# Kernel tuning notes

Hardware: AMD Instinct MI355X
Metric: run time of the kernel (lower is better)

## Reference

```python
import jax, jax.numpy as jnp
import numpy as np

B, T, IN = 256, 512, 4      # batch, seq_len, input dim
M, D, NS = 3, 256, 64       # n kaarma models, dictionary size, state dim
H = 128                     # controller (GRU) hidden size
GU, GS = 0.5, 0.5           # gaussian kernel widths (input / state)


def setup_inputs() -> dict:
    key = jax.random.key(0)
    ks = jax.random.split(key, 12)
    s = lambda k, shp, sc: (jax.random.normal(k, shp, dtype=jnp.float32) * sc)
    return {
        "x": s(ks[0], (B, T, IN), 1.0),
        "y": s(ks[1], (B, T), 1.0),
        # MKAARMA: per-model dictionary (inputs U, states S) and coefficients A
        "U": s(ks[2], (M, D, IN), 1.0),
        "S": s(ks[3], (M, D, NS), 0.3),
        "A": s(ks[4], (M, D, NS), 1.0 / np.sqrt(D)),
        # GRU controller (input dim = M + 1 error channel)
        "W_ih": s(ks[5], (M + 1, 3 * H), 1.0 / np.sqrt(M + 1)),
        "W_hh": s(ks[6], (H, 3 * H), 1.0 / np.sqrt(H)),
        "b_ih": s(ks[7], (3 * H,), 0.1),
        "b_hh": s(ks[8], (3 * H,), 0.1),
        # linear_decode: (H-1) -> M gate logits
        "Wd": s(ks[9], (H - 1, M), 1.0 / np.sqrt(H - 1)),
        "bd": s(ks[10], (M,), 0.1),
    }


def _forward(x, y, U, S, A, W_ih, W_hh, b_ih, b_hh, Wd, bd):
    init_gate = jnp.array([[0.3333, 0.3333, 0.3334]], dtype=x.dtype)

    def step(carry, xs):
        s, h, gate_prev, err = carry          # [B,NS], [B,H], [B,M], [B]
        x_t, y_t = xs                         # [B,IN], [B]
        # --- mkaarma: gaussian input*state kernel against dictionary ---
        du = jnp.sum((x_t[:, None, None, :] - U[None]) ** 2, axis=-1)  # [B,M,D]
        ds = jnp.sum((s[:, None, None, :] - S[None]) ** 2, axis=-1)   # [B,M,D]
        K = jnp.exp(-GU * du - GS * ds)                                # [B,M,D]
        new_state = jnp.einsum('bmd,mdn->bmn', K, A)                   # [B,M,NS]
        encoded = jnp.max(K, axis=-1)                                  # [B,M]
        # --- controller: GRU cell on [similarities, error] ---
        inp = jnp.concatenate([encoded, err[:, None]], axis=1)         # [B,M+1]
        gi = inp @ W_ih + b_ih
        gh = h @ W_hh + b_hh
        ir, iz, inn = jnp.split(gi, 3, axis=1)
        hr, hz, hn = jnp.split(gh, 3, axis=1)
        r = jax.nn.sigmoid(ir + hr)
        z = jax.nn.sigmoid(iz + hz)
        n = jnp.tanh(inn + r * hn)
        h_new = (1.0 - z) * n + z * h                                  # [B,H]
        # --- gate decode + theta blend ---
        gate = jax.nn.softmax(h_new[:, :-1] @ Wd + bd, axis=1)          # [B,M]
        theta = jax.nn.sigmoid(h_new[:, -1:])                           # [B,1]
        gate = gate * theta + gate_prev * (1.0 - theta)
        s_new = jnp.einsum('bm,bmn->bn', gate, new_state)               # [B,NS]
        pred = s_new[:, -1]                                             # [B]
        err_new = pred - y_t
        penalty = jnp.sum(gate * (1.0 - gate), axis=1, keepdims=True)   # [B,1]
        return (s_new, h_new, gate, err_new), (pred, penalty)

    carry0 = (
        jnp.zeros((x.shape[0], NS), x.dtype),
        jnp.zeros((x.shape[0], H), x.dtype),
        jnp.tile(init_gate, (x.shape[0], 1)),
        jnp.ones((x.shape[0],), x.dtype),
    )
    xs = (jnp.swapaxes(x, 0, 1), jnp.swapaxes(y, 0, 1))  # time-major
    _, (o, p) = jax.lax.scan(step, carry0, xs)
    return jnp.swapaxes(o, 0, 1), jnp.swapaxes(p, 0, 1)   # [B,T], [B,T,1]


def reference(x, y, U, S, A, W_ih, W_hh, b_ih, b_hh, Wd, bd):
    return _forward(x, y, U, S, A, W_ih, W_hh, b_ih, b_hh, Wd, bd)
```

## Files before the change

kernel.cpp:

```cpp
#include <hip/hip_runtime.h>
#include <math.h>

constexpr int kB  = 256;
constexpr int kT  = 512;
constexpr int kNS = 64;
constexpr int kH  = 128;

constexpr int kWRowsLds = 256;
constexpr int kWPad     = 132;

__device__ __forceinline__ float sigmoidf_(float v) { return 1.0f / (1.0f + __expf(-v)); }
__device__ __forceinline__ float dot4(float4 a, float4 b) {
    return a.x*b.x + a.y*b.y + a.z*b.z + a.w*b.w;
}

template <int CTRL>
__device__ __forceinline__ float dppf(float x) {
    return __int_as_float(__builtin_amdgcn_mov_dpp(__float_as_int(x), CTRL, 0xf, 0xf, true));
}
__device__ __forceinline__ float red_max64(float x) {
    x = fmaxf(x, dppf<0xB1>(x));
    x = fmaxf(x, dppf<0x4E>(x));
    x = fmaxf(x, dppf<0x124>(x));
    x = fmaxf(x, dppf<0x128>(x));
    x = fmaxf(x, __shfl_xor(x, 16, 64));
    x = fmaxf(x, __shfl_xor(x, 32, 64));
    return x;
}
__device__ __forceinline__ float red_sum64(float x) {
    x += dppf<0xB1>(x);
    x += dppf<0x4E>(x);
    x += dppf<0x124>(x);
    x += dppf<0x128>(x);
    x += __shfl_xor(x, 16, 64);
    x += __shfl_xor(x, 32, 64);
    return x;
}

extern "C" __global__ void __launch_bounds__(256)
whh_transpose(const float* __restrict__ Whh, float* __restrict__ WhhT) {
    const int o = blockIdx.x * 256 + threadIdx.x;
    const int j = o >> 7, k = o & 127;
    WhhT[o] = Whh[k * 384 + j];
}

extern "C" __global__ void __launch_bounds__(512, 2)
disc_kernel(const float* __restrict__ x,   const float* __restrict__ y,
            const float* __restrict__ U,   const float* __restrict__ S,
            const float* __restrict__ A,   const float* __restrict__ Wih,
            const float* __restrict__ bih, const float* __restrict__ bhh,
            const float* __restrict__ Wd,  const float* __restrict__ bd,
            const float* __restrict__ WhhT,
            float* __restrict__ out_o,  float* __restrict__ out_p)
{
    const int b    = blockIdx.x;
    const int tid  = threadIdx.x;
    const int lane = tid & 63;
    const int wid  = tid >> 6;
    const int hb   = tid & 1;

    __shared__ __align__(16) float sh_K[768];
    __shared__ __align__(16) float sh_part[512];
    __shared__ __align__(16) float sh_part2[512];
    __shared__ __align__(16) float sh_gh[384];
    __shared__ __align__(16) float sh_h[2][kH];
    __shared__ __align__(16) float sh_s[kNS];
    __shared__ __align__(16) float sh_Wih[4 * 384];
    __shared__ __align__(16) float sh_bih[384];
    __shared__ __align__(16) float sh_bhh[384];
    __shared__ float sh_Wd[384];
    __shared__ float sh_bd[4];
    __shared__ float sh_encA[8];
    __shared__ float sh_encB[8];
    __shared__ __align__(16) float sh_xt[4];
    __shared__ float sh_x2, sh_s2, sh_err;
    __shared__ float sh_yt[2];
    __shared__ __align__(16) float sh_W[kWRowsLds * kWPad];

    const float4* S4 = reinterpret_cast<const float4*>(S);
    const float4* U4 = reinterpret_cast<const float4*>(U);

    float4 Sa[16]; float4 Ua; float Ca;
    float4 Sb[8];  float Ub0, Ub1; float Cb;
    {
        float ss = 0.f;
#pragma unroll
        for (int j = 0; j < 16; ++j) { Sa[j] = S4[tid * 16 + j]; ss += dot4(Sa[j], Sa[j]); }
        Ua = U4[tid];
        Ca = -0.5f * (dot4(Ua, Ua) + ss);
    }
    const int pbrow = 512 + (tid >> 1);
    {
        float ss = 0.f;
#pragma unroll
        for (int j = 0; j < 8; ++j) { Sb[j] = S4[pbrow * 16 + hb * 8 + j]; ss += dot4(Sb[j], Sb[j]); }
        Ub0 = U[pbrow * 4 + hb * 2 + 0];
        Ub1 = U[pbrow * 4 + hb * 2 + 1];
        Cb = -0.5f * (Ub0*Ub0 + Ub1*Ub1 + ss);
    }
    float A1[64];
#pragma unroll
    for (int dd = 0; dd < 64; ++dd)
        A1[dd] = A[((wid >> 2) * 256 + (wid & 3) * 64 + dd) * 64 + lane];
    float A2[32];
#pragma unroll
    for (int dd = 0; dd < 32; ++dd)
        A2[dd] = A[(512 + (wid >> 1) * 64 + (wid & 1) * 32 + dd) * 64 + lane];

    float g0 = 0.3333f, g1 = 0.3333f, g2 = 0.3334f;

    for (int i = tid; i < 1536; i += 512) sh_Wih[i] = Wih[i];
    for (int i = tid; i < 384; i += 512) {
        sh_bih[i] = bih[i];
        sh_bhh[i] = bhh[i];
        sh_gh[i]  = bhh[i];
        sh_Wd[i]  = (i < 381) ? Wd[i] : 0.f;
    }
    for (int i4 = tid; i4 < kWRowsLds * 32; i4 += 512) {
        const int r = i4 >> 5, c4 = i4 & 31;
        reinterpret_cast<float4*>(sh_W + r * kWPad)[c4] =
            reinterpret_cast<const float4*>(WhhT)[i4];
    }
    if (tid < 3) sh_bd[tid] = bd[tid];
    if (tid < kNS) sh_s[tid] = 0.f;
    if (tid < kH)  { sh_h[0][tid] = 0.f; sh_h[1][tid] = 0.f; }
    if (tid == 0) {
        sh_err = 1.0f; sh_s2 = 0.f;
        float4 xv = reinterpret_cast<const float4*>(x)[(size_t)b * kT];
        reinterpret_cast<float4*>(sh_xt)[0] = xv;
        sh_x2 = dot4(xv, xv);
        sh_yt[0] = y[(size_t)b * kT];
    }
    __syncthreads();

    for (int t = 0; t < kT; ++t) {
        const int par  = t & 1;
        const int par1 = (t + 1) & 1;

        if (wid >= 1 && wid <= 4) {
            const int u = tid - 64;
            const float4* W4 = reinterpret_cast<const float4*>(sh_W + u * kWPad);
            const float4* h4 = reinterpret_cast<const float4*>(sh_h[par]);
            float g = 0.f;
#pragma unroll 4
            for (int k4 = 16; k4 < 32; ++k4)
                g += dot4(h4[k4], W4[k4]);
            sh_gh[u] += g;
        } else if (wid == 5 || wid == 6) {
            const int u = 256 + (tid - 320);
            const float4* W4 = reinterpret_cast<const float4*>(WhhT) + u * 32;
            const float4* h4 = reinterpret_cast<const float4*>(sh_h[par]);
            float g = 0.f;
#pragma unroll 4
            for (int k4 = 24; k4 < 32; ++k4)
                g += dot4(h4[k4], W4[k4]);
            sh_gh[u] += g;
        }
        {
            const float scal = -0.5f * (sh_x2 + sh_s2);
            const float4 xt4 = reinterpret_cast<const float4*>(sh_xt)[0];
            const float4* s4 = reinterpret_cast<const float4*>(sh_s);
            float da0 = 0.f, da1 = 0.f, dblo = 0.f, dbhi = 0.f;
#pragma unroll
            for (int j = 0; j < 8; ++j) {
                const float4 sv0 = s4[j];
                const float4 sv1 = s4[8 + j];
                da0  += dot4(sv0, Sa[j]);
                da1  += dot4(sv1, Sa[8 + j]);
                dblo += dot4(sv0, Sb[j]);
                dbhi += dot4(sv1, Sb[j]);
            }
            const float db = hb ? dbhi : dblo;
            const float kk_a = __expf(scal + Ca + dot4(xt4, Ua) + da0 + da1);
            const float xbp  = hb ? (xt4.z*Ub0 + xt4.w*Ub1) : (xt4.x*Ub0 + xt4.y*Ub1);
            const float ph   = db + Cb + xbp;
            const float po   = dppf<0xB1>(ph);
            const float kk_b = __expf(scal + ph + po);
            sh_K[tid] = kk_a;
            if (hb == 0) sh_K[512 + (tid >> 1)] = kk_b;
            const float mA = red_max64(kk_a);
            const float mB = red_max64(kk_b);
            if (lane == 0) { sh_encA[wid] = mA; sh_encB[wid] = mB; }
        }
        __syncthreads();

        {
            const float4* K4 = reinterpret_cast<const float4*>(sh_K + wid * 64);
            float acc = 0.f;
#pragma unroll
            for (int j = 0; j < 16; ++j) {
                const float4 kv = K4[j];
                acc += kv.x*A1[4*j] + kv.y*A1[4*j+1] + kv.z*A1[4*j+2] + kv.w*A1[4*j+3];
            }
            sh_part[tid] = acc;
            const float4* K4b = reinterpret_cast<const float4*>(
                                    sh_K + 512 + (wid >> 1) * 64 + (wid & 1) * 32);
            float accb = 0.f;
#pragma unroll
            for (int j = 0; j < 8; ++j) {
                const float4 kv = K4b[j];
                accb += kv.x*A2[4*j] + kv.y*A2[4*j+1] + kv.z*A2[4*j+2] + kv.w*A2[4*j+3];
            }
            sh_part2[tid] = accb;
        }
        if (tid < 128) {
            const float e0 = fmaxf(fmaxf(sh_encA[0], sh_encA[1]), fmaxf(sh_encA[2], sh_encA[3]));
            const float e1 = fmaxf(fmaxf(sh_encA[4], sh_encA[5]), fmaxf(sh_encA[6], sh_encA[7]));
            const float e2 = fmaxf(fmaxf(fmaxf(sh_encB[0], sh_encB[1]), fmaxf(sh_encB[2], sh_encB[3])),
                                   fmaxf(fmaxf(sh_encB[4], sh_encB[5]), fmaxf(sh_encB[6], sh_encB[7])));
            const float er = sh_err;
            const int j = tid;
            const float gir = sh_bih[j]       + e0*sh_Wih[j]        + e1*sh_Wih[384 + j]
                                              + e2*sh_Wih[768 + j]  + er*sh_Wih[1152 + j];
            const float giz = sh_bih[128 + j] + e0*sh_Wih[128 + j]  + e1*sh_Wih[512 + j]
                                              + e2*sh_Wih[896 + j]  + er*sh_Wih[1280 + j];
            const float gin = sh_bih[256 + j] + e0*sh_Wih[256 + j]  + e1*sh_Wih[640 + j]
                                              + e2*sh_Wih[1024 + j] + er*sh_Wih[1408 + j];
            const float r  = sigmoidf_(gir + sh_gh[j]);
            const float z  = sigmoidf_(giz + sh_gh[128 + j]);
            const float nn = tanhf(gin + r * sh_gh[256 + j]);
            sh_h[par1][j] = (1.f - z) * nn + z * sh_h[par][j];
        }
        __syncthreads();

        if (wid == 0) {
            const float hA = sh_h[par1][lane];
            const float hB = sh_h[par1][64 + lane];
            const float theta = sigmoidf_(sh_h[par1][127]);
            float l0 = hA * sh_Wd[lane*3+0] + hB * sh_Wd[(64+lane)*3+0];
            float l1 = hA * sh_Wd[lane*3+1] + hB * sh_Wd[(64+lane)*3+1];
            float l2 = hA * sh_Wd[lane*3+2] + hB * sh_Wd[(64+lane)*3+2];
            l0 = red_sum64(l0);
            l1 = red_sum64(l1);
            l2 = red_sum64(l2);
            l0 += sh_bd[0]; l1 += sh_bd[1]; l2 += sh_bd[2];
            const float mx = fmaxf(l0, fmaxf(l1, l2));
            const float x0 = __expf(l0 - mx), x1 = __expf(l1 - mx), x2 = __expf(l2 - mx);
            const float inv = theta / (x0 + x1 + x2);
            const float omt = 1.f - theta;
            g0 = x0*inv + g0*omt;
            g1 = x1*inv + g1*omt;
            g2 = x2*inv + g2*omt;
            const float ns0 = (sh_part[lane]       + sh_part[64 + lane])
                            + (sh_part[128 + lane] + sh_part[192 + lane]);
            const float ns1 = (sh_part[256 + lane] + sh_part[320 + lane])
                            + (sh_part[384 + lane] + sh_part[448 + lane]);
            const float ns2 = ((sh_part2[lane]       + sh_part2[64 + lane])
                            +  (sh_part2[128 + lane] + sh_part2[192 + lane]))
                            + ((sh_part2[256 + lane] + sh_part2[320 + lane])
                            +  (sh_part2[384 + lane] + sh_part2[448 + lane]));
            const float sn = g0*ns0 + g1*ns1 + g2*ns2;
            sh_s[lane] = sn;
            if (lane == 0)
                out_p[(size_t)b * kT + t] = g0*(1.f-g0) + g1*(1.f-g1) + g2*(1.f-g2);
            if (lane == 63) {
                out_o[(size_t)b * kT + t] = sn;
                sh_err = sn - sh_yt[par];
            }
            const float ss = red_sum64(sn * sn);
            if (lane == 0) sh_s2 = ss;
        } else if (wid <= 4) {
            const int u = tid - 64;
            const float4* W4 = reinterpret_cast<const float4*>(sh_W + u * kWPad);
            const float4* h4 = reinterpret_cast<const float4*>(sh_h[par1]);
            float g = sh_bhh[u];
#pragma unroll 8
            for (int k4 = 0; k4 < 16; ++k4)
                g += dot4(h4[k4], W4[k4]);
            sh_gh[u] = g;
        } else if (wid <= 6) {
            const int u = 256 + (tid - 320);
            const float4* W4 = reinterpret_cast<const float4*>(WhhT) + u * 32;
            const float4* h4 = reinterpret_cast<const float4*>(sh_h[par1]);
            float g = sh_bhh[u];
#pragma unroll 8
            for (int k4 = 0; k4 < 24; ++k4)
                g += dot4(h4[k4], W4[k4]);
            sh_gh[u] = g;
        } else {
            if (lane == 0 && (t + 1) < kT) {
                float4 xv = reinterpret_cast<const float4*>(x)[(size_t)b * kT + t + 1];
                reinterpret_cast<float4*>(sh_xt)[0] = xv;
                sh_x2 = dot4(xv, xv);
                sh_yt[par1] = y[(size_t)b * kT + t + 1];
            }
        }
        __syncthreads();
    }
}

extern "C" void kernel_launch(void* const* d_in, const int* in_sizes, int n_in,
                              void* d_out, int out_size, void* d_ws, size_t ws_size,
                              hipStream_t stream)
{
    const float* x   = (const float*)d_in[0];
    const float* y   = (const float*)d_in[1];
    const float* U   = (const float*)d_in[2];
    const float* S   = (const float*)d_in[3];
    const float* A   = (const float*)d_in[4];
    const float* Wih = (const float*)d_in[5];
    const float* Whh = (const float*)d_in[6];
    const float* bih = (const float*)d_in[7];
    const float* bhh = (const float*)d_in[8];
    const float* Wd  = (const float*)d_in[9];
    const float* bd  = (const float*)d_in[10];

    float* WhhT  = (float*)d_ws;
    float* out_o = (float*)d_out;
    float* out_p = out_o + kB * kT;

    hipLaunchKernelGGL(whh_transpose, dim3(192), dim3(256), 0, stream, Whh, WhhT);
    hipLaunchKernelGGL(disc_kernel, dim3(kB), dim3(512), 0, stream,
                       x, y, U, S, A, Wih, bih, bhh, Wd, bd, WhhT, out_o, out_p);
}
```

Before: 2.655 ms.

## Widen block to 768 threads, one dictionary entry per thread, simplify GRU split

```diff
diff --git a/kernel.cpp b/kernel.cpp
--- a/kernel.cpp
+++ b/kernel.cpp
@@ -5,6 +5,7 @@
 constexpr int kT  = 512;
 constexpr int kNS = 64;
 constexpr int kH  = 128;
+constexpr int kNT = 768;
 
 constexpr int kWRowsLds = 256;
 constexpr int kWPad     = 132;
@@ -44,7 +45,7 @@
     WhhT[o] = Whh[k * 384 + j];
 }
 
-extern "C" __global__ void __launch_bounds__(512, 2)
+extern "C" __global__ void __launch_bounds__(768, 3)
 disc_kernel(const float* __restrict__ x,   const float* __restrict__ y,
             const float* __restrict__ U,   const float* __restrict__ S,
             const float* __restrict__ A,   const float* __restrict__ Wih,
@@ -57,21 +58,19 @@
     const int tid  = threadIdx.x;
     const int lane = tid & 63;
     const int wid  = tid >> 6;
-    const int hb   = tid & 1;
 
     __shared__ __align__(16) float sh_K[768];
-    __shared__ __align__(16) float sh_part[512];
-    __shared__ __align__(16) float sh_part2[512];
-    __shared__ __align__(16) float sh_gh[384];
-    __shared__ __align__(16) float sh_h[2][kH];
+    __shared__ __align__(16) float sh_part[768];
+    __shared__ __align__(16) float sh_gh[256];
+    __shared__ __align__(16) float sh_ghn[2][128];
+    __shared__ __align__(16) float sh_h[kH];
     __shared__ __align__(16) float sh_s[kNS];
     __shared__ __align__(16) float sh_Wih[4 * 384];
     __shared__ __align__(16) float sh_bih[384];
     __shared__ __align__(16) float sh_bhh[384];
     __shared__ float sh_Wd[384];
     __shared__ float sh_bd[4];
-    __shared__ float sh_encA[8];
-    __shared__ float sh_encB[8];
+    __shared__ float sh_enc[12];
     __shared__ __align__(16) float sh_xt[4];
     __shared__ float sh_x2, sh_s2, sh_err;
     __shared__ float sh_yt[2];
@@ -81,7 +80,6 @@
     const float4* U4 = reinterpret_cast<const float4*>(U);
 
     float4 Sa[16]; float4 Ua; float Ca;
-    float4 Sb[8];  float Ub0, Ub1; float Cb;
     {
         float ss = 0.f;
 #pragma unroll
@@ -89,41 +87,28 @@
         Ua = U4[tid];
         Ca = -0.5f * (dot4(Ua, Ua) + ss);
     }
-    const int pbrow = 512 + (tid >> 1);
-    {
-        float ss = 0.f;
-#pragma unroll
-        for (int j = 0; j < 8; ++j) { Sb[j] = S4[pbrow * 16 + hb * 8 + j]; ss += dot4(Sb[j], Sb[j]); }
-        Ub0 = U[pbrow * 4 + hb * 2 + 0];
-        Ub1 = U[pbrow * 4 + hb * 2 + 1];
-        Cb = -0.5f * (Ub0*Ub0 + Ub1*Ub1 + ss);
-    }
     float A1[64];
 #pragma unroll
     for (int dd = 0; dd < 64; ++dd)
-        A1[dd] = A[((wid >> 2) * 256 + (wid & 3) * 64 + dd) * 64 + lane];
-    float A2[32];
-#pragma unroll
-    for (int dd = 0; dd < 32; ++dd)
-        A2[dd] = A[(512 + (wid >> 1) * 64 + (wid & 1) * 32 + dd) * 64 + lane];
+        A1[dd] = A[(wid * 64 + dd) * 64 + lane];
 
     float g0 = 0.3333f, g1 = 0.3333f, g2 = 0.3334f;
 
-    for (int i = tid; i < 1536; i += 512) sh_Wih[i] = Wih[i];
-    for (int i = tid; i < 384; i += 512) {
+    for (int i = tid; i < 1536; i += kNT) sh_Wih[i] = Wih[i];
+    for (int i = tid; i < 384; i += kNT) {
         sh_bih[i] = bih[i];
         sh_bhh[i] = bhh[i];
-        sh_gh[i]  = bhh[i];
         sh_Wd[i]  = (i < 381) ? Wd[i] : 0.f;
     }
-    for (int i4 = tid; i4 < kWRowsLds * 32; i4 += 512) {
+    for (int i = tid; i < 256; i += kNT) sh_gh[i] = bhh[i];
+    if (tid < 128) { sh_ghn[0][tid] = 0.f; sh_ghn[1][tid] = 0.f; sh_h[tid] = 0.f; }
+    for (int i4 = tid; i4 < kWRowsLds * 32; i4 += kNT) {
         const int r = i4 >> 5, c4 = i4 & 31;
         reinterpret_cast<float4*>(sh_W + r * kWPad)[c4] =
             reinterpret_cast<const float4*>(WhhT)[i4];
     }
     if (tid < 3) sh_bd[tid] = bd[tid];
     if (tid < kNS) sh_s[tid] = 0.f;
-    if (tid < kH)  { sh_h[0][tid] = 0.f; sh_h[1][tid] = 0.f; }
     if (tid == 0) {
         sh_err = 1.0f; sh_s2 = 0.f;
         float4 xv = reinterpret_cast<const float4*>(x)[(size_t)b * kT];
@@ -137,77 +122,38 @@
         const int par  = t & 1;
         const int par1 = (t + 1) & 1;
 
-        if (wid >= 1 && wid <= 4) {
-            const int u = tid - 64;
-            const float4* W4 = reinterpret_cast<const float4*>(sh_W + u * kWPad);
-            const float4* h4 = reinterpret_cast<const float4*>(sh_h[par]);
-            float g = 0.f;
-#pragma unroll 4
-            for (int k4 = 16; k4 < 32; ++k4)
-                g += dot4(h4[k4], W4[k4]);
-            sh_gh[u] += g;
-        } else if (wid == 5 || wid == 6) {
-            const int u = 256 + (tid - 320);
-            const float4* W4 = reinterpret_cast<const float4*>(WhhT) + u * 32;
-            const float4* h4 = reinterpret_cast<const float4*>(sh_h[par]);
-            float g = 0.f;
-#pragma unroll 4
-            for (int k4 = 24; k4 < 32; ++k4)
-                g += dot4(h4[k4], W4[k4]);
-            sh_gh[u] += g;
-        }
         {
             const float scal = -0.5f * (sh_x2 + sh_s2);
             const float4 xt4 = reinterpret_cast<const float4*>(sh_xt)[0];
             const float4* s4 = reinterpret_cast<const float4*>(sh_s);
-            float da0 = 0.f, da1 = 0.f, dblo = 0.f, dbhi = 0.f;
+            float da0 = 0.f, da1 = 0.f;
 #pragma unroll
             for (int j = 0; j < 8; ++j) {
-                const float4 sv0 = s4[j];
-                const float4 sv1 = s4[8 + j];
-                da0  += dot4(sv0, Sa[j]);
-                da1  += dot4(sv1, Sa[8 + j]);
-                dblo += dot4(sv0, Sb[j]);
-                dbhi += dot4(sv1, Sb[j]);
-            }
-            const float db = hb ? dbhi : dblo;
-            const float kk_a = __expf(scal + Ca + dot4(xt4, Ua) + da0 + da1);
-            const float xbp  = hb ? (xt4.z*Ub0 + xt4.w*Ub1) : (xt4.x*Ub0 + xt4.y*Ub1);
-            const float ph   = db + Cb + xbp;
-            const float po   = dppf<0xB1>(ph);
-            const float kk_b = __expf(scal + ph + po);
-            sh_K[tid] = kk_a;
-            if (hb == 0) sh_K[512 + (tid >> 1)] = kk_b;
-            const float mA = red_max64(kk_a);
-            const float mB = red_max64(kk_b);
-            if (lane == 0) { sh_encA[wid] = mA; sh_encB[wid] = mB; }
+                da0 += dot4(s4[j],     Sa[j]);
+                da1 += dot4(s4[8 + j], Sa[8 + j]);
+            }
+            const float kk = __expf(scal + Ca + dot4(xt4, Ua) + da0 + da1);
+            sh_K[tid] = kk;
+            const float m = red_max64(kk);
+            if (lane == 0) sh_enc[wid] = m;
         }
         __syncthreads();
 
         {
             const float4* K4 = reinterpret_cast<const float4*>(sh_K + wid * 64);
-            float acc = 0.f;
-#pragma unroll
-            for (int j = 0; j < 16; ++j) {
-                const float4 kv = K4[j];
-                acc += kv.x*A1[4*j] + kv.y*A1[4*j+1] + kv.z*A1[4*j+2] + kv.w*A1[4*j+3];
-            }
-            sh_part[tid] = acc;
-            const float4* K4b = reinterpret_cast<const float4*>(
-                                    sh_K + 512 + (wid >> 1) * 64 + (wid & 1) * 32);
-            float accb = 0.f;
-#pragma unroll
-            for (int j = 0; j < 8; ++j) {
-                const float4 kv = K4b[j];
-                accb += kv.x*A2[4*j] + kv.y*A2[4*j+1] + kv.z*A2[4*j+2] + kv.w*A2[4*j+3];
-            }
-            sh_part2[tid] = accb;
+            float acc0 = 0.f, acc1 = 0.f;
+#pragma unroll
+            for (int j = 0; j < 16; j += 2) {
+                const float4 k0 = K4[j], k1 = K4[j + 1];
+                acc0 += k0.x*A1[4*j]   + k0.y*A1[4*j+1] + k0.z*A1[4*j+2] + k0.w*A1[4*j+3];
+                acc1 += k1.x*A1[4*j+4] + k1.y*A1[4*j+5] + k1.z*A1[4*j+6] + k1.w*A1[4*j+7];
+            }
+            sh_part[tid] = acc0 + acc1;
         }
         if (tid < 128) {
-            const float e0 = fmaxf(fmaxf(sh_encA[0], sh_encA[1]), fmaxf(sh_encA[2], sh_encA[3]));
-            const float e1 = fmaxf(fmaxf(sh_encA[4], sh_encA[5]), fmaxf(sh_encA[6], sh_encA[7]));
-            const float e2 = fmaxf(fmaxf(fmaxf(sh_encB[0], sh_encB[1]), fmaxf(sh_encB[2], sh_encB[3])),
-                                   fmaxf(fmaxf(sh_encB[4], sh_encB[5]), fmaxf(sh_encB[6], sh_encB[7])));
+            const float e0 = fmaxf(fmaxf(sh_enc[0], sh_enc[1]),  fmaxf(sh_enc[2],  sh_enc[3]));
+            const float e1 = fmaxf(fmaxf(sh_enc[4], sh_enc[5]),  fmaxf(sh_enc[6],  sh_enc[7]));
+            const float e2 = fmaxf(fmaxf(sh_enc[8], sh_enc[9]),  fmaxf(sh_enc[10], sh_enc[11]));
             const float er = sh_err;
             const int j = tid;
             const float gir = sh_bih[j]       + e0*sh_Wih[j]        + e1*sh_Wih[384 + j]
@@ -216,17 +162,18 @@
                                               + e2*sh_Wih[896 + j]  + er*sh_Wih[1280 + j];
             const float gin = sh_bih[256 + j] + e0*sh_Wih[256 + j]  + e1*sh_Wih[640 + j]
                                               + e2*sh_Wih[1024 + j] + er*sh_Wih[1408 + j];
+            const float hn_ = sh_bhh[256 + j] + sh_ghn[0][j] + sh_ghn[1][j];
             const float r  = sigmoidf_(gir + sh_gh[j]);
             const float z  = sigmoidf_(giz + sh_gh[128 + j]);
-            const float nn = tanhf(gin + r * sh_gh[256 + j]);
-            sh_h[par1][j] = (1.f - z) * nn + z * sh_h[par][j];
+            const float nn = tanhf(gin + r * hn_);
+            sh_h[j] = (1.f - z) * nn + z * sh_h[j];
         }
         __syncthreads();
 
         if (wid == 0) {
-            const float hA = sh_h[par1][lane];
-            const float hB = sh_h[par1][64 + lane];
-            const float theta = sigmoidf_(sh_h[par1][127]);
+            const float hA = sh_h[lane];
+            const float hB = sh_h[64 + lane];
+            const float theta = sigmoidf_(sh_h[127]);
             float l0 = hA * sh_Wd[lane*3+0] + hB * sh_Wd[(64+lane)*3+0];
             float l1 = hA * sh_Wd[lane*3+1] + hB * sh_Wd[(64+lane)*3+1];
             float l2 = hA * sh_Wd[lane*3+2] + hB * sh_Wd[(64+lane)*3+2];
@@ -245,10 +192,8 @@
                             + (sh_part[128 + lane] + sh_part[192 + lane]);
             const float ns1 = (sh_part[256 + lane] + sh_part[320 + lane])
                             + (sh_part[384 + lane] + sh_part[448 + lane]);
-            const float ns2 = ((sh_part2[lane]       + sh_part2[64 + lane])
-                            +  (sh_part2[128 + lane] + sh_part2[192 + lane]))
-                            + ((sh_part2[256 + lane] + sh_part2[320 + lane])
-                            +  (sh_part2[384 + lane] + sh_part2[448 + lane]));
+            const float ns2 = (sh_part[512 + lane] + sh_part[576 + lane])
+                            + (sh_part[640 + lane] + sh_part[704 + lane]);
             const float sn = g0*ns0 + g1*ns1 + g2*ns2;
             sh_s[lane] = sn;
             if (lane == 0)
@@ -259,31 +204,37 @@
             }
             const float ss = red_sum64(sn * sn);
             if (lane == 0) sh_s2 = ss;
-        } else if (wid <= 4) {
-            const int u = tid - 64;
-            const float4* W4 = reinterpret_cast<const float4*>(sh_W + u * kWPad);
-            const float4* h4 = reinterpret_cast<const float4*>(sh_h[par1]);
-            float g = sh_bhh[u];
-#pragma unroll 8
-            for (int k4 = 0; k4 < 16; ++k4)
-                g += dot4(h4[k4], W4[k4]);
-            sh_gh[u] = g;
-        } else if (wid <= 6) {
-            const int u = 256 + (tid - 320);
-            const float4* W4 = reinterpret_cast<const float4*>(WhhT) + u * 32;
-            const float4* h4 = reinterpret_cast<const float4*>(sh_h[par1]);
-            float g = sh_bhh[u];
-#pragma unroll 8
-            for (int k4 = 0; k4 < 24; ++k4)
-                g += dot4(h4[k4], W4[k4]);
-            sh_gh[u] = g;
-        } else {
+        } else if (wid == 1) {
             if (lane == 0 && (t + 1) < kT) {
                 float4 xv = reinterpret_cast<const float4*>(x)[(size_t)b * kT + t + 1];
                 reinterpret_cast<float4*>(sh_xt)[0] = xv;
                 sh_x2 = dot4(xv, xv);
                 sh_yt[par1] = y[(size_t)b * kT + t + 1];
             }
+        } else if (wid < 6) {
+            const int u = tid - 128;
+            const float4* W4 = reinterpret_cast<const float4*>(sh_W + u * kWPad);
+            const float4* h4 = reinterpret_cast<const float4*>(sh_h);
+            float ga = sh_bhh[u], gb = 0.f;
+#pragma unroll 8
+            for (int k4 = 0; k4 < 32; k4 += 2) {
+                ga += dot4(h4[k4],     W4[k4]);
+                gb += dot4(h4[k4 + 1], W4[k4 + 1]);
+            }
+            sh_gh[u] = ga + gb;
+        } else if (wid < 10) {
+            const int v    = tid - 384;
+            const int u    = 256 + (v >> 1);
+            const int half = v & 1;
+            const float4* W4 = reinterpret_cast<const float4*>(WhhT) + u * 32 + half * 16;
+            const float4* h4 = reinterpret_cast<const float4*>(sh_h) + half * 16;
+            float ga = 0.f, gb = 0.f;
+#pragma unroll 8
+            for (int k4 = 0; k4 < 16; k4 += 2) {
+                ga += dot4(h4[k4],     W4[k4]);
+                gb += dot4(h4[k4 + 1], W4[k4 + 1]);
+            }
+            sh_ghn[half][u - 256] = ga + gb;
         }
         __syncthreads();
     }
@@ -310,6 +261,6 @@
     float* out_p = out_o + kB * kT;
 
     hipLaunchKernelGGL(whh_transpose, dim3(192), dim3(256), 0, stream, Whh, WhhT);
-    hipLaunchKernelGGL(disc_kernel, dim3(kB), dim3(512), 0, stream,
+    hipLaunchKernelGGL(disc_kernel, dim3(kB), dim3(kNT), 0, stream,
                        x, y, U, S, A, Wih, bih, bhh, Wd, bd, WhhT, out_o, out_p);
 }
```

New measurement: 2.672 ms. Within noise of the previous version (+0.6%).

## Replicate gate/state tail across warps to drop one barrier per timestep

Applied to the files above, without the earlier changes.

```diff
diff --git a/kernel.cpp b/kernel.cpp
--- a/kernel.cpp
+++ b/kernel.cpp
@@ -10,6 +10,9 @@
 constexpr int kWPad     = 132;
 
 __device__ __forceinline__ float sigmoidf_(float v) { return 1.0f / (1.0f + __expf(-v)); }
+__device__ __forceinline__ float tanhf_(float v) {
+    return 1.0f - 2.0f / (1.0f + __expf(2.0f * v));
+}
 __device__ __forceinline__ float dot4(float4 a, float4 b) {
     return a.x*b.x + a.y*b.y + a.z*b.z + a.w*b.w;
 }
@@ -63,8 +66,8 @@
     __shared__ __align__(16) float sh_part[512];
     __shared__ __align__(16) float sh_part2[512];
     __shared__ __align__(16) float sh_gh[384];
-    __shared__ __align__(16) float sh_h[2][kH];
-    __shared__ __align__(16) float sh_s[kNS];
+    __shared__ __align__(16) float sh_h[kH];
+    __shared__ __align__(16) float sh_sW[8][kNS];
     __shared__ __align__(16) float sh_Wih[4 * 384];
     __shared__ __align__(16) float sh_bih[384];
     __shared__ __align__(16) float sh_bhh[384];
@@ -72,8 +75,7 @@
     __shared__ float sh_bd[4];
     __shared__ float sh_encA[8];
     __shared__ float sh_encB[8];
-    __shared__ __align__(16) float sh_xt[4];
-    __shared__ float sh_x2, sh_s2, sh_err;
+    __shared__ __align__(16) float sh_xt[2][4];
     __shared__ float sh_yt[2];
     __shared__ __align__(16) float sh_W[kWRowsLds * kWPad];
 
@@ -108,6 +110,7 @@
         A2[dd] = A[(512 + (wid >> 1) * 64 + (wid & 1) * 32 + dd) * 64 + lane];
 
     float g0 = 0.3333f, g1 = 0.3333f, g2 = 0.3334f;
+    float err = 1.0f, s2 = 0.f;
 
     for (int i = tid; i < 1536; i += 512) sh_Wih[i] = Wih[i];
     for (int i = tid; i < 384; i += 512) {
@@ -121,45 +124,62 @@
         reinterpret_cast<float4*>(sh_W + r * kWPad)[c4] =
             reinterpret_cast<const float4*>(WhhT)[i4];
     }
+    sh_sW[wid][lane] = 0.f;
     if (tid < 3) sh_bd[tid] = bd[tid];
-    if (tid < kNS) sh_s[tid] = 0.f;
-    if (tid < kH)  { sh_h[0][tid] = 0.f; sh_h[1][tid] = 0.f; }
+    if (tid < kH) sh_h[tid] = 0.f;
     if (tid == 0) {
-        sh_err = 1.0f; sh_s2 = 0.f;
         float4 xv = reinterpret_cast<const float4*>(x)[(size_t)b * kT];
-        reinterpret_cast<float4*>(sh_xt)[0] = xv;
-        sh_x2 = dot4(xv, xv);
+        reinterpret_cast<float4*>(sh_xt[0])[0] = xv;
         sh_yt[0] = y[(size_t)b * kT];
     }
     __syncthreads();
 
+    auto tail_step = [&](int tp) {
+        const float hA = sh_h[lane];
+        const float hB = sh_h[64 + lane];
+        const float theta = sigmoidf_(sh_h[127]);
+        float l0 = hA * sh_Wd[lane*3+0] + hB * sh_Wd[(64+lane)*3+0];
+        float l1 = hA * sh_Wd[lane*3+1] + hB * sh_Wd[(64+lane)*3+1];
+        float l2 = hA * sh_Wd[lane*3+2] + hB * sh_Wd[(64+lane)*3+2];
+        l0 = red_sum64(l0) + sh_bd[0];
+        l1 = red_sum64(l1) + sh_bd[1];
+        l2 = red_sum64(l2) + sh_bd[2];
+        const float mx = fmaxf(l0, fmaxf(l1, l2));
+        const float x0 = __expf(l0 - mx), x1 = __expf(l1 - mx), x2e = __expf(l2 - mx);
+        const float inv = theta / (x0 + x1 + x2e);
+        const float omt = 1.f - theta;
+        g0 = x0*inv + g0*omt;
+        g1 = x1*inv + g1*omt;
+        g2 = x2e*inv + g2*omt;
+        const float ns0 = (sh_part[lane]       + sh_part[64 + lane])
+                        + (sh_part[128 + lane] + sh_part[192 + lane]);
+        const float ns1 = (sh_part[256 + lane] + sh_part[320 + lane])
+                        + (sh_part[384 + lane] + sh_part[448 + lane]);
+        const float ns2 = ((sh_part2[lane]       + sh_part2[64 + lane])
+                        +  (sh_part2[128 + lane] + sh_part2[192 + lane]))
+                        + ((sh_part2[256 + lane] + sh_part2[320 + lane])
+                        +  (sh_part2[384 + lane] + sh_part2[448 + lane]));
+        const float sn = g0*ns0 + g1*ns1 + g2*ns2;
+        sh_sW[wid][lane] = sn;
+        if (wid == 0) {
+            if (lane == 0)
+                out_p[(size_t)b * kT + tp] = g0*(1.f-g0) + g1*(1.f-g1) + g2*(1.f-g2);
+            if (lane == 63)
+                out_o[(size_t)b * kT + tp] = sn;
+        }
+        err = __shfl(sn, 63, 64) - sh_yt[tp & 1];
+        s2  = red_sum64(sn * sn);
+    };
+
     for (int t = 0; t < kT; ++t) {
-        const int par  = t & 1;
-        const int par1 = (t + 1) & 1;
-
-        if (wid >= 1 && wid <= 4) {
-            const int u = tid - 64;
-            const float4* W4 = reinterpret_cast<const float4*>(sh_W + u * kWPad);
-            const float4* h4 = reinterpret_cast<const float4*>(sh_h[par]);
-            float g = 0.f;
-#pragma unroll 4
-            for (int k4 = 16; k4 < 32; ++k4)
-                g += dot4(h4[k4], W4[k4]);
-            sh_gh[u] += g;
-        } else if (wid == 5 || wid == 6) {
-            const int u = 256 + (tid - 320);
-            const float4* W4 = reinterpret_cast<const float4*>(WhhT) + u * 32;
-            const float4* h4 = reinterpret_cast<const float4*>(sh_h[par]);
-            float g = 0.f;
-#pragma unroll 4
-            for (int k4 = 24; k4 < 32; ++k4)
-                g += dot4(h4[k4], W4[k4]);
-            sh_gh[u] += g;
-        }
+        const int cur = t & 1;
+
+        if (t > 0) tail_step(t - 1);
         {
-            const float scal = -0.5f * (sh_x2 + sh_s2);
-            const float4 xt4 = reinterpret_cast<const float4*>(sh_xt)[0];
-            const float4* s4 = reinterpret_cast<const float4*>(sh_s);
+            const float4 xt4 = reinterpret_cast<const float4*>(sh_xt[cur])[0];
+            const float xx2 = dot4(xt4, xt4);
+            const float scal = -0.5f * (xx2 + s2);
+            const float4* s4 = reinterpret_cast<const float4*>(sh_sW[wid]);
             float da0 = 0.f, da1 = 0.f, dblo = 0.f, dbhi = 0.f;
 #pragma unroll
             for (int j = 0; j < 8; ++j) {
@@ -182,6 +202,29 @@
             const float mB = red_max64(kk_b);
             if (lane == 0) { sh_encA[wid] = mA; sh_encB[wid] = mB; }
         }
+        if (wid >= 1 && wid <= 4) {
+            const int u = tid - 64;
+            const float4* W4 = reinterpret_cast<const float4*>(sh_W + u * kWPad);
+            const float4* h4 = reinterpret_cast<const float4*>(sh_h);
+            float ga = sh_bhh[u], gb = 0.f;
+#pragma unroll 8
+            for (int k4 = 0; k4 < 32; k4 += 2) {
+                ga += dot4(h4[k4],     W4[k4]);
+                gb += dot4(h4[k4 + 1], W4[k4 + 1]);
+            }
+            sh_gh[u] = ga + gb;
+        } else if (wid == 5 || wid == 6) {
+            const int u = 256 + (tid - 320);
+            const float4* W4 = reinterpret_cast<const float4*>(WhhT) + u * 32;
+            const float4* h4 = reinterpret_cast<const float4*>(sh_h);
+            float ga = sh_bhh[u], gb = 0.f;
+#pragma unroll 8
+            for (int k4 = 0; k4 < 32; k4 += 2) {
+                ga += dot4(h4[k4],     W4[k4]);
+                gb += dot4(h4[k4 + 1], W4[k4 + 1]);
+            }
+            sh_gh[u] = ga + gb;
+        }
         __syncthreads();
 
         {
@@ -208,7 +251,7 @@
             const float e1 = fmaxf(fmaxf(sh_encA[4], sh_encA[5]), fmaxf(sh_encA[6], sh_encA[7]));
             const float e2 = fmaxf(fmaxf(fmaxf(sh_encB[0], sh_encB[1]), fmaxf(sh_encB[2], sh_encB[3])),
                                    fmaxf(fmaxf(sh_encB[4], sh_encB[5]), fmaxf(sh_encB[6], sh_encB[7])));
-            const float er = sh_err;
+            const float er = err;
             const int j = tid;
             const float gir = sh_bih[j]       + e0*sh_Wih[j]        + e1*sh_Wih[384 + j]
                                               + e2*sh_Wih[768 + j]  + er*sh_Wih[1152 + j];
@@ -218,75 +261,18 @@
                                               + e2*sh_Wih[1024 + j] + er*sh_Wih[1408 + j];
             const float r  = sigmoidf_(gir + sh_gh[j]);
             const float z  = sigmoidf_(giz + sh_gh[128 + j]);
-            const float nn = tanhf(gin + r * sh_gh[256 + j]);
-            sh_h[par1][j] = (1.f - z) * nn + z * sh_h[par][j];
+            const float nn = tanhf_(gin + r * sh_gh[256 + j]);
+            sh_h[j] = (1.f - z) * nn + z * sh_h[j];
+        }
+        if (wid == 7 && lane == 0 && (t + 1) < kT) {
+            float4 xv = reinterpret_cast<const float4*>(x)[(size_t)b * kT + t + 1];
+            reinterpret_cast<float4*>(sh_xt[(t + 1) & 1])[0] = xv;
+            sh_yt[(t + 1) & 1] = y[(size_t)b * kT + t + 1];
         }
         __syncthreads();
-
-        if (wid == 0) {
-            const float hA = sh_h[par1][lane];
-            const float hB = sh_h[par1][64 + lane];
-            const float theta = sigmoidf_(sh_h[par1][127]);
-            float l0 = hA * sh_Wd[lane*3+0] + hB * sh_Wd[(64+lane)*3+0];
-            float l1 = hA * sh_Wd[lane*3+1] + hB * sh_Wd[(64+lane)*3+1];
-            float l2 = hA * sh_Wd[lane*3+2] + hB * sh_Wd[(64+lane)*3+2];
-            l0 = red_sum64(l0);
-            l1 = red_sum64(l1);
-            l2 = red_sum64(l2);
-            l0 += sh_bd[0]; l1 += sh_bd[1]; l2 += sh_bd[2];
-            const float mx = fmaxf(l0, fmaxf(l1, l2));
-            const float x0 = __expf(l0 - mx), x1 = __expf(l1 - mx), x2 = __expf(l2 - mx);
-            const float inv = theta / (x0 + x1 + x2);
-            const float omt = 1.f - theta;
-            g0 = x0*inv + g0*omt;
-            g1 = x1*inv + g1*omt;
-            g2 = x2*inv + g2*omt;
-            const float ns0 = (sh_part[lane]       + sh_part[64 + lane])
-                            + (sh_part[128 + lane] + sh_part[192 + lane]);
-            const float ns1 = (sh_part[256 + lane] + sh_part[320 + lane])
-                            + (sh_part[384 + lane] + sh_part[448 + lane]);
-            const float ns2 = ((sh_part2[lane]       + sh_part2[64 + lane])
-                            +  (sh_part2[128 + lane] + sh_part2[192 + lane]))
-                            + ((sh_part2[256 + lane] + sh_part2[320 + lane])
-                            +  (sh_part2[384 + lane] + sh_part2[448 + lane]));
-            const float sn = g0*ns0 + g1*ns1 + g2*ns2;
-            sh_s[lane] = sn;
-            if (lane == 0)
-                out_p[(size_t)b * kT + t] = g0*(1.f-g0) + g1*(1.f-g1) + g2*(1.f-g2);
-            if (lane == 63) {
-                out_o[(size_t)b * kT + t] = sn;
-                sh_err = sn - sh_yt[par];
-            }
-            const float ss = red_sum64(sn * sn);
-            if (lane == 0) sh_s2 = ss;
-        } else if (wid <= 4) {
-            const int u = tid - 64;
-            const float4* W4 = reinterpret_cast<const float4*>(sh_W + u * kWPad);
-            const float4* h4 = reinterpret_cast<const float4*>(sh_h[par1]);
-            float g = sh_bhh[u];
-#pragma unroll 8
-            for (int k4 = 0; k4 < 16; ++k4)
-                g += dot4(h4[k4], W4[k4]);
-            sh_gh[u] = g;
-        } else if (wid <= 6) {
-            const int u = 256 + (tid - 320);
-            const float4* W4 = reinterpret_cast<const float4*>(WhhT) + u * 32;
-            const float4* h4 = reinterpret_cast<const float4*>(sh_h[par1]);
-            float g = sh_bhh[u];
-#pragma unroll 8
-            for (int k4 = 0; k4 < 24; ++k4)
-                g += dot4(h4[k4], W4[k4]);
-            sh_gh[u] = g;
-        } else {
-            if (lane == 0 && (t + 1) < kT) {
-                float4 xv = reinterpret_cast<const float4*>(x)[(size_t)b * kT + t + 1];
-                reinterpret_cast<float4*>(sh_xt)[0] = xv;
-                sh_x2 = dot4(xv, xv);
-                sh_yt[par1] = y[(size_t)b * kT + t + 1];
-            }
-        }
-        __syncthreads();
-    }
+    }
+
+    tail_step(kT - 1);
 }
 
 extern "C" void kernel_launch(void* const* d_in, const int* in_sizes, int n_in,
```

Result: slower. 2.878 ms (+8.4%).
